# Optimization experiments

Measured on AMD Instinct MI355X. Metric: run time of the kernel, lower is better.

The kernel has to match this reference:

```python
import jax, jax.numpy as jnp
import numpy as np

B, T, I, H, O, L = 128, 512, 64, 256, 2, 2


def _gru_layer(x_seq, w_ih, w_hh, b_ih, b_hh):
    # x_seq: [B, T, in], w_ih: [3H, in], w_hh: [3H, H], biases: [3H]
    # PyTorch gate order: r, z, n
    xg = jnp.einsum('bti,gi->btg', x_seq, w_ih) + b_ih  # [B, T, 3H]
    h0 = jnp.zeros((x_seq.shape[0], w_hh.shape[1]), x_seq.dtype)

    def step(h, xg_t):
        hg = h @ w_hh.T + b_hh  # [B, 3H]
        xr, xz, xn = jnp.split(xg_t, 3, axis=-1)
        hr, hz, hn = jnp.split(hg, 3, axis=-1)
        r = jax.nn.sigmoid(xr + hr)
        z = jax.nn.sigmoid(xz + hz)
        n = jnp.tanh(xn + r * hn)
        h_new = (1.0 - z) * n + z * h
        return h_new, h_new

    _, hs = jax.lax.scan(step, h0, jnp.swapaxes(xg, 0, 1))  # [T, B, H]
    return jnp.swapaxes(hs, 0, 1)  # [B, T, H]


def setup_inputs() -> dict:
    key = jax.random.key(0)
    ks = jax.random.split(key, 12)
    s_ih0 = 1.0 / np.sqrt(H)
    inp = {
        'x': jax.random.normal(ks[0], (B, T, I), jnp.float32),
        'w_ih0': jax.random.uniform(ks[1], (3 * H, I), jnp.float32, -s_ih0, s_ih0),
        'w_hh0': jax.random.uniform(ks[2], (3 * H, H), jnp.float32, -s_ih0, s_ih0),
        'b_ih0': jax.random.uniform(ks[3], (3 * H,), jnp.float32, -s_ih0, s_ih0),
        'b_hh0': jax.random.uniform(ks[4], (3 * H,), jnp.float32, -s_ih0, s_ih0),
        'w_ih1': jax.random.uniform(ks[5], (3 * H, H), jnp.float32, -s_ih0, s_ih0),
        'w_hh1': jax.random.uniform(ks[6], (3 * H, H), jnp.float32, -s_ih0, s_ih0),
        'b_ih1': jax.random.uniform(ks[7], (3 * H,), jnp.float32, -s_ih0, s_ih0),
        'b_hh1': jax.random.uniform(ks[8], (3 * H,), jnp.float32, -s_ih0, s_ih0),
        'fc_w': jax.random.uniform(ks[9], (O, H), jnp.float32, -s_ih0, s_ih0),
        'fc_b': jax.random.uniform(ks[10], (O,), jnp.float32, -s_ih0, s_ih0),
    }
    return inp


def reference(x, w_ih0, w_hh0, b_ih0, b_hh0, w_ih1, w_hh1, b_ih1, b_hh1, fc_w, fc_b):
    h1 = _gru_layer(x, w_ih0, w_hh0, b_ih0, b_hh0)   # [B, T, H]
    h2 = _gru_layer(h1, w_ih1, w_hh1, b_ih1, b_hh1)  # [B, T, H]
    last = jax.nn.relu(h2[:, -1])                     # [B, H]
    return last @ fc_w.T + fc_b                       # [B, O]
```

## Files before the change

### kernel.cpp

```cpp
#include <hip/hip_runtime.h>


namespace {
constexpr int kB = 128, kT = 512, kI = 64, kH = 256, kBH = kB * kH;
constexpr int NG = 8, GW = 32, RPG = 16, NWG = 256, NT = 512;

constexpr int SRS = 36;
constexpr int SKS = 16 * SRS + 4;
constexpr int O_S0 = 0;
constexpr int O_S1 = O_S0 + 8 * SKS;
constexpr int O_X  = O_S1 + 8 * SKS;
constexpr int O_PB = O_X + RPG * 68;
constexpr int PBN  = 4 * 16 * 36;
constexpr int LDSF = O_PB + PBN;

constexpr int kFlagStride = 16;
}

__device__ __forceinline__ float sigf(float v) { return 1.0f / (1.0f + expf(-v)); }
__device__ __forceinline__ float dot4(const float4 a, const float4 b) {
  return a.x * b.x + a.y * b.y + a.z * b.z + a.w * b.w;
}
__device__ __forceinline__ float red8(float v) {
  v += __shfl_xor(v, 8);
  v += __shfl_xor(v, 16);
  v += __shfl_xor(v, 32);
  return v;
}
#define F4(p) (*(const float4*)(p))

__global__ __launch_bounds__(NT, 2) void gru_persistent(
    const float* __restrict__ x,
    const float* __restrict__ wih0, const float* __restrict__ whh0,
    const float* __restrict__ bih0, const float* __restrict__ bhh0,
    const float* __restrict__ wih1, const float* __restrict__ whh1,
    const float* __restrict__ bih1, const float* __restrict__ bhh1,
    const float* __restrict__ fcw, const float* __restrict__ fcb,
    float* __restrict__ h0buf, float* __restrict__ h1buf,
    unsigned* flags, float* __restrict__ out)
{
  __shared__ float lds[LDSF];

  const int bid = blockIdx.x;
  const int g   = bid >> 5;
  const int wg  = bid & (GW - 1);
  const int tid = threadIdx.x;
  const int r0  = g * RPG;
  const int j0  = wg * 8;

  const int wave = tid >> 6;
  const int lane = tid & 63;
  const int lay  = wave >> 2;
  const int fam  = (wave >> 1) & 1;
  const int rh   = wave & 1;
  const int ju   = lane & 7;
  const int ks   = lane >> 3;
  const int jg   = j0 + ju;

  for (int i = tid; i < PBN; i += NT) lds[O_PB + i] = 0.f;

  float4 wr0[8], wr1[8], wr2[8];
  if (lay == 0) {
    if (fam == 0) {
#define L0F0(wrg, gg) { \
      const float* wi = wih0 + (size_t)((gg) * kH + jg) * kI + ks * 8;   \
      const float* wh = whh0 + (size_t)((gg) * kH + jg) * kH + ks * 32;  \
      wrg[0] = F4(wi); wrg[1] = F4(wi + 4);                              \
      wrg[2] = F4(wh); wrg[3] = F4(wh + 4); wrg[4] = F4(wh + 8); }
      L0F0(wr0, 0) L0F0(wr1, 1) L0F0(wr2, 2)
    } else {
#define L0F1(wrg, gg) { \
      const float* wh = whh0 + (size_t)((gg) * kH + jg) * kH + ks * 32 + 12; \
      wrg[0] = F4(wh); wrg[1] = F4(wh + 4); wrg[2] = F4(wh + 8);             \
      wrg[3] = F4(wh + 12); wrg[4] = F4(wh + 16); }
      L0F1(wr0, 0) L0F1(wr1, 1) L0F1(wr2, 2)
    }
  } else {
    const float* ws = fam ? whh1 : wih1;
#define L1W(wrg, gg) { \
    const float* wp = ws + (size_t)((gg) * kH + jg) * kH + ks * 32;          \
    wrg[0] = F4(wp);      wrg[1] = F4(wp + 4);  wrg[2] = F4(wp + 8);         \
    wrg[3] = F4(wp + 12); wrg[4] = F4(wp + 16); wrg[5] = F4(wp + 20);        \
    wrg[6] = F4(wp + 24); wrg[7] = F4(wp + 28); }
    L1W(wr0, 0) L1W(wr1, 1) L1W(wr2, 2)
  }

  float fb_r = 0.f, fb_z = 0.f, fb_ni = 0.f, fb_nh = 0.f;
  if (tid < 256) {
    const int layf = tid >> 7, uf = tid & 7, jf = j0 + uf;
    const float* bi = layf ? bih1 : bih0;
    const float* bh = layf ? bhh1 : bhh0;
    fb_r  = bi[jf] + bh[jf];
    fb_z  = bi[kH + jf] + bh[kH + jf];
    fb_ni = bi[2 * kH + jf];
    fb_nh = bh[2 * kH + jf];
  }

  unsigned* myflag = flags + (unsigned)((g << 5) + (tid & 31)) * kFlagStride;

  __syncthreads();

  for (int s = 0; s <= kT; ++s) {
    {
      const float* h0p = h0buf + (size_t)((s + 1) & 1) * kBH;
      const float* h1p = h1buf + (size_t)(s & 1) * kBH;
      #pragma unroll
      for (int p = 0; p < 4; ++p) {
        const int i  = tid + p * NT;
        const int ro = i >> 7, k2 = i & 127;
        const int k  = k2 * 2, ksg = k >> 5, off = k & 31;
        const unsigned long long v0 = __hip_atomic_load(
            (const unsigned long long*)(h0p + (size_t)(r0 + ro) * kH) + k2,
            __ATOMIC_RELAXED, __HIP_MEMORY_SCOPE_AGENT);
        const unsigned long long v1 = __hip_atomic_load(
            (const unsigned long long*)(h1p + (size_t)(r0 + ro) * kH) + k2,
            __ATOMIC_RELAXED, __HIP_MEMORY_SCOPE_AGENT);
        float2 f0, f1;
        __builtin_memcpy(&f0, &v0, 8);
        __builtin_memcpy(&f1, &v1, 8);
        *(float2*)(lds + O_S0 + ksg * SKS + ro * SRS + off) = f0;
        *(float2*)(lds + O_S1 + ksg * SKS + ro * SRS + off) = f1;
      }
      if (s < kT && tid < 256) {
        const int ro = tid >> 4, c4 = (tid & 15) * 4;
        *(float4*)(lds + O_X + ro * 68 + c4) =
            F4(x + (size_t)(r0 + ro) * kT * kI + (size_t)s * kI + c4);
      }
    }
    __syncthreads();

    const bool wact = lay ? (s >= 1) : (s < kT);
    if (wact) {
      float prr[8], pzz[8], pni[8], pnh[8];
      #pragma unroll
      for (int r = 0; r < 8; ++r) {
        const int ro = rh * 8 + r;
        float pr = 0.f, pz = 0.f, pxi = 0.f, pxh = 0.f;
        if (lay == 0) {
          if (fam == 0) {
            const float* ax = lds + O_X + ro * 68 + ks * 8;
            const float4 x0 = F4(ax), x1 = F4(ax + 4);
            pr  += dot4(x0, wr0[0]) + dot4(x1, wr0[1]);
            pz  += dot4(x0, wr1[0]) + dot4(x1, wr1[1]);
            pxi += dot4(x0, wr2[0]) + dot4(x1, wr2[1]);
            const float* ah = lds + O_S0 + ks * SKS + ro * SRS;
            #pragma unroll
            for (int i = 0; i < 3; ++i) {
              const float4 hv = F4(ah + i * 4);
              pr  += dot4(hv, wr0[2 + i]);
              pz  += dot4(hv, wr1[2 + i]);
              pxh += dot4(hv, wr2[2 + i]);
            }
          } else {
            const float* ah = lds + O_S0 + ks * SKS + ro * SRS + 12;
            #pragma unroll
            for (int i = 0; i < 5; ++i) {
              const float4 hv = F4(ah + i * 4);
              pr  += dot4(hv, wr0[i]);
              pz  += dot4(hv, wr1[i]);
              pxh += dot4(hv, wr2[i]);
            }
          }
        } else {
          const float* aa = lds + (fam ? O_S1 : O_S0) + ks * SKS + ro * SRS;
          #pragma unroll
          for (int i = 0; i < 8; ++i) {
            const float4 av = F4(aa + i * 4);
            pr += dot4(av, wr0[i]);
            pz += dot4(av, wr1[i]);
            if (fam) pxh += dot4(av, wr2[i]);
            else     pxi += dot4(av, wr2[i]);
          }
        }
        prr[r] = pr; pzz[r] = pz; pni[r] = pxi; pnh[r] = pxh;
      }
      #pragma unroll
      for (int r = 0; r < 8; ++r) { prr[r] = red8(prr[r]); pzz[r] = red8(pzz[r]); }
      if (lay == 0 && fam == 0) {
        #pragma unroll
        for (int r = 0; r < 8; ++r) { pni[r] = red8(pni[r]); pnh[r] = red8(pnh[r]); }
      } else if (fam == 0) {
        #pragma unroll
        for (int r = 0; r < 8; ++r) pni[r] = red8(pni[r]);
      } else {
        #pragma unroll
        for (int r = 0; r < 8; ++r) pnh[r] = red8(pnh[r]);
      }
      if (ks == 0) {
        #pragma unroll
        for (int r = 0; r < 8; ++r) {
          float* pb = lds + O_PB + ((wave >> 1) * 16 + rh * 8 + r) * SRS + ju;
          pb[0] = prr[r]; pb[8] = pzz[r];
          if (lay == 0 && fam == 0) { pb[16] = pni[r]; pb[24] = pnh[r]; }
          else if (fam == 0)          pb[16] = pni[r];
          else                        pb[24] = pnh[r];
        }
      }
    }
    __syncthreads();

    if (tid < 256) {
      const int layf = tid >> 7;
      const bool act = layf ? (s >= 1) : (s < kT);
      if (act) {
        const int rof = (tid >> 3) & 15, uf = tid & 7, jf = j0 + uf;
        const float* p0 = lds + O_PB + ((layf * 2) * 16 + rof) * SRS + uf;
        const float* p1 = p0 + 16 * SRS;
        const float rr = sigf(p0[0] + p1[0] + fb_r);
        const float zz = sigf(p0[8] + p1[8] + fb_z);
        const float nn = tanhf(p0[16] + p1[16] + fb_ni +
                               rr * (p0[24] + p1[24] + fb_nh));
        const float hp = lds[(layf ? O_S1 : O_S0) +
                             (jf >> 5) * SKS + rof * SRS + (jf & 31)];
        const float hv = (1.f - zz) * nn + zz * hp;
        float* hout = layf ? (h1buf + (size_t)((s + 1) & 1) * kBH)
                           : (h0buf + (size_t)(s & 1) * kBH);
        __hip_atomic_store(hout + (size_t)(r0 + rof) * kH + jf, hv,
                           __ATOMIC_RELAXED, __HIP_MEMORY_SCOPE_AGENT);
      }
    }
    __syncthreads();

    if (tid == 0) {
      __hip_atomic_store(flags + (unsigned)bid * kFlagStride,
                         (unsigned)(s + 1),
                         __ATOMIC_RELAXED, __HIP_MEMORY_SCOPE_AGENT);
    }
    while (__hip_atomic_load(myflag, __ATOMIC_RELAXED,
                             __HIP_MEMORY_SCOPE_AGENT) < (unsigned)(s + 1)) {
      __builtin_amdgcn_s_sleep(1);
    }
    asm volatile("" ::: "memory");
  }

  if (wg == 0 && tid < 256) {
    const int rv = tid >> 4, o = (tid >> 3) & 1, kseg = tid & 7;
    const float* hf = h1buf + (size_t)kBH + (size_t)(r0 + rv) * kH;
    const float* wfc = fcw + (size_t)o * kH;
    float acc = 0.f;
    #pragma unroll 8
    for (int k = kseg * 32; k < kseg * 32 + 32; ++k) {
      const float hv = __hip_atomic_load(hf + k, __ATOMIC_RELAXED,
                                         __HIP_MEMORY_SCOPE_AGENT);
      acc += fmaxf(hv, 0.f) * wfc[k];
    }
    acc += __shfl_xor(acc, 1);
    acc += __shfl_xor(acc, 2);
    acc += __shfl_xor(acc, 4);
    if (kseg == 0) out[(r0 + rv) * 2 + o] = acc + fcb[o];
  }
}

extern "C" void kernel_launch(void* const* d_in, const int* in_sizes, int n_in,
                              void* d_out, int out_size, void* d_ws, size_t ws_size,
                              hipStream_t stream) {
  const float* x    = (const float*)d_in[0];
  const float* wih0 = (const float*)d_in[1];
  const float* whh0 = (const float*)d_in[2];
  const float* bih0 = (const float*)d_in[3];
  const float* bhh0 = (const float*)d_in[4];
  const float* wih1 = (const float*)d_in[5];
  const float* whh1 = (const float*)d_in[6];
  const float* bih1 = (const float*)d_in[7];
  const float* bhh1 = (const float*)d_in[8];
  const float* fcw  = (const float*)d_in[9];
  const float* fcb  = (const float*)d_in[10];

  float* h0buf = (float*)d_ws;
  float* h1buf = h0buf + 2 * kBH;
  unsigned* flags = (unsigned*)(h1buf + 2 * kBH);
  float* out = (float*)d_out;

  hipMemsetAsync(d_ws, 0,
                 (size_t)(4 * kBH) * sizeof(float) +
                 (size_t)NWG * kFlagStride * sizeof(unsigned), stream);

  gru_persistent<<<NWG, NT, 0, stream>>>(
      x, wih0, whh0, bih0, bhh0, wih1, whh1, bih1, bhh1,
      fcw, fcb, h0buf, h1buf, flags, out);
}
```

Before: 3.779 ms.

## Replace per-step flag barrier with tagged hidden-state words and triple buffering

Removes the end-of-step flag barrier that every workgroup spun on. Each stored hidden value now carries a 2-bit step tag in its low mantissa bits, and readers poll the data itself until the tags match. A third buffer slot lets producers run ahead, and a looser lagged flag only guards against slot reuse. This trades a full group barrier per step for data-driven waiting, at the cost of two bits of float precision and spin-polling on global loads.

After: 3.470 ms. 1.09x faster.

```diff
diff --git a/kernel.cpp b/kernel.cpp
--- a/kernel.cpp
+++ b/kernel.cpp
@@ -14,8 +14,10 @@
 constexpr int PBN  = 4 * 16 * 36;
 constexpr int LDSF = O_PB + PBN;
 
-constexpr int kFlagStride = 16;
-}
+constexpr int FS = 16;
+}
+
+using ull = unsigned long long;
 
 __device__ __forceinline__ float sigf(float v) { return 1.0f / (1.0f + expf(-v)); }
 __device__ __forceinline__ float dot4(const float4 a, const float4 b) {
@@ -36,8 +38,10 @@
     const float* __restrict__ wih1, const float* __restrict__ whh1,
     const float* __restrict__ bih1, const float* __restrict__ bhh1,
     const float* __restrict__ fcw, const float* __restrict__ fcb,
-    float* __restrict__ h0buf, float* __restrict__ h1buf,
-    unsigned* flags, float* __restrict__ out)
+    unsigned* __restrict__ h0w,
+    unsigned* __restrict__ h1w,
+    unsigned* __restrict__ sd,
+    float* __restrict__ out)
 {
   __shared__ float lds[LDSF];
 
@@ -96,38 +100,80 @@
     fb_nh = bh[2 * kH + jf];
   }
 
-  unsigned* myflag = flags + (unsigned)((g << 5) + (tid & 31)) * kFlagStride;
+  int RO[4], K2[4];
+  #pragma unroll
+  for (int p = 0; p < 4; ++p) {
+    const int i = tid + p * NT;
+    RO[p] = i >> 7; K2[p] = i & 127;
+  }
 
   __syncthreads();
 
   for (int s = 0; s <= kT; ++s) {
+    const int slot0 = (s + 2) % 3;
+    const int slot1 = (s + 1) % 3;
+    const unsigned e0 = (unsigned)(s & 3);
+    const unsigned e1 = (unsigned)((s - 1) & 3);
+
+    if (s < kT && tid < 256) {
+      const int ro = tid >> 4, c4 = (tid & 15) * 4;
+      *(float4*)(lds + O_X + ro * 68 + c4) =
+          F4(x + (size_t)(r0 + ro) * kT * kI + (size_t)s * kI + c4);
+    }
+    if (s >= 2 && tid >= 480) {
+      const unsigned* f = sd + (unsigned)((g << 5) + (tid - 480)) * FS;
+      while (__hip_atomic_load(f, __ATOMIC_RELAXED, __HIP_MEMORY_SCOPE_AGENT)
+             < (unsigned)(s - 1)) { }
+    }
+
+    ull v0[4], v1[4];
     {
-      const float* h0p = h0buf + (size_t)((s + 1) & 1) * kBH;
-      const float* h1p = h1buf + (size_t)(s & 1) * kBH;
+      const ull* A0[4]; const ull* A1[4];
       #pragma unroll
       for (int p = 0; p < 4; ++p) {
-        const int i  = tid + p * NT;
-        const int ro = i >> 7, k2 = i & 127;
-        const int k  = k2 * 2, ksg = k >> 5, off = k & 31;
-        const unsigned long long v0 = __hip_atomic_load(
-            (const unsigned long long*)(h0p + (size_t)(r0 + ro) * kH) + k2,
-            __ATOMIC_RELAXED, __HIP_MEMORY_SCOPE_AGENT);
-        const unsigned long long v1 = __hip_atomic_load(
-            (const unsigned long long*)(h1p + (size_t)(r0 + ro) * kH) + k2,
-            __ATOMIC_RELAXED, __HIP_MEMORY_SCOPE_AGENT);
-        float2 f0, f1;
-        __builtin_memcpy(&f0, &v0, 8);
-        __builtin_memcpy(&f1, &v1, 8);
-        *(float2*)(lds + O_S0 + ksg * SKS + ro * SRS + off) = f0;
+        A0[p] = (const ull*)(h0w + (size_t)slot0 * kBH +
+                             (size_t)(r0 + RO[p]) * kH) + K2[p];
+        A1[p] = (const ull*)(h1w + (size_t)slot1 * kBH +
+                             (size_t)(r0 + RO[p]) * kH) + K2[p];
+      }
+      for (;;) {
+        #pragma unroll
+        for (int p = 0; p < 4; ++p)
+          v0[p] = __hip_atomic_load(A0[p], __ATOMIC_RELAXED,
+                                    __HIP_MEMORY_SCOPE_AGENT);
+        if (s >= 1) {
+          #pragma unroll
+          for (int p = 0; p < 4; ++p)
+            v1[p] = __hip_atomic_load(A1[p], __ATOMIC_RELAXED,
+                                      __HIP_MEMORY_SCOPE_AGENT);
+        }
+        unsigned bad = 0;
+        #pragma unroll
+        for (int p = 0; p < 4; ++p)
+          bad |= ((unsigned)v0[p] ^ e0) | ((unsigned)(v0[p] >> 32) ^ e0);
+        if (s >= 1) {
+          #pragma unroll
+          for (int p = 0; p < 4; ++p)
+            bad |= ((unsigned)v1[p] ^ e1) | ((unsigned)(v1[p] >> 32) ^ e1);
+        }
+        if (!(bad & 3u)) break;
+      }
+    }
+    #pragma unroll
+    for (int p = 0; p < 4; ++p) {
+      const int ksg = K2[p] >> 4, off = (K2[p] * 2) & 31, ro = RO[p];
+      float2 f0; __builtin_memcpy(&f0, &v0[p], 8);
+      *(float2*)(lds + O_S0 + ksg * SKS + ro * SRS + off) = f0;
+      if (s >= 1) {
+        float2 f1; __builtin_memcpy(&f1, &v1[p], 8);
         *(float2*)(lds + O_S1 + ksg * SKS + ro * SRS + off) = f1;
       }
-      if (s < kT && tid < 256) {
-        const int ro = tid >> 4, c4 = (tid & 15) * 4;
-        *(float4*)(lds + O_X + ro * 68 + c4) =
-            F4(x + (size_t)(r0 + ro) * kT * kI + (size_t)s * kI + c4);
-      }
     }
     __syncthreads();
+    if (tid == 0) {
+      __hip_atomic_store(sd + (unsigned)bid * FS, (unsigned)(s + 1),
+                         __ATOMIC_RELAXED, __HIP_MEMORY_SCOPE_AGENT);
+    }
 
     const bool wact = lay ? (s >= 1) : (s < kT);
     if (wact) {
@@ -213,36 +259,31 @@
         const float hp = lds[(layf ? O_S1 : O_S0) +
                              (jf >> 5) * SKS + rof * SRS + (jf & 31)];
         const float hv = (1.f - zz) * nn + zz * hp;
-        float* hout = layf ? (h1buf + (size_t)((s + 1) & 1) * kBH)
-                           : (h0buf + (size_t)(s & 1) * kBH);
-        __hip_atomic_store(hout + (size_t)(r0 + rof) * kH + jf, hv,
-                           __ATOMIC_RELAXED, __HIP_MEMORY_SCOPE_AGENT);
+        const int slot = layf ? ((s - 1) % 3) : (s % 3);
+        const unsigned tag = layf ? (unsigned)(s & 3) : (unsigned)((s + 1) & 3);
+        const unsigned bits = (__float_as_uint(hv) & ~3u) | tag;
+        unsigned* hw = (layf ? h1w : h0w) + (size_t)slot * kBH +
+                       (size_t)(r0 + rof) * kH + jf;
+        __hip_atomic_store(hw, bits, __ATOMIC_RELAXED,
+                           __HIP_MEMORY_SCOPE_AGENT);
       }
     }
     __syncthreads();
-
-    if (tid == 0) {
-      __hip_atomic_store(flags + (unsigned)bid * kFlagStride,
-                         (unsigned)(s + 1),
-                         __ATOMIC_RELAXED, __HIP_MEMORY_SCOPE_AGENT);
-    }
-    while (__hip_atomic_load(myflag, __ATOMIC_RELAXED,
-                             __HIP_MEMORY_SCOPE_AGENT) < (unsigned)(s + 1)) {
-      __builtin_amdgcn_s_sleep(1);
-    }
-    asm volatile("" ::: "memory");
   }
 
   if (wg == 0 && tid < 256) {
     const int rv = tid >> 4, o = (tid >> 3) & 1, kseg = tid & 7;
-    const float* hf = h1buf + (size_t)kBH + (size_t)(r0 + rv) * kH;
+    const unsigned* hf = h1w + (size_t)((kT - 1) % 3) * kBH +
+                         (size_t)(r0 + rv) * kH;
     const float* wfc = fcw + (size_t)o * kH;
     float acc = 0.f;
-    #pragma unroll 8
     for (int k = kseg * 32; k < kseg * 32 + 32; ++k) {
-      const float hv = __hip_atomic_load(hf + k, __ATOMIC_RELAXED,
-                                         __HIP_MEMORY_SCOPE_AGENT);
-      acc += fmaxf(hv, 0.f) * wfc[k];
+      unsigned b;
+      do {
+        b = __hip_atomic_load(hf + k, __ATOMIC_RELAXED,
+                              __HIP_MEMORY_SCOPE_AGENT);
+      } while ((b & 3u) != (unsigned)(kT & 3));
+      acc += fmaxf(__uint_as_float(b), 0.f) * wfc[k];
     }
     acc += __shfl_xor(acc, 1);
     acc += __shfl_xor(acc, 2);
@@ -266,16 +307,16 @@
   const float* fcw  = (const float*)d_in[9];
   const float* fcb  = (const float*)d_in[10];
 
-  float* h0buf = (float*)d_ws;
-  float* h1buf = h0buf + 2 * kBH;
-  unsigned* flags = (unsigned*)(h1buf + 2 * kBH);
+  unsigned* h0w = (unsigned*)d_ws;
+  unsigned* h1w = h0w + 3 * kBH;
+  unsigned* sd  = h1w + 3 * kBH;
   float* out = (float*)d_out;
 
   hipMemsetAsync(d_ws, 0,
-                 (size_t)(4 * kBH) * sizeof(float) +
-                 (size_t)NWG * kFlagStride * sizeof(unsigned), stream);
+                 (size_t)(6 * kBH) * sizeof(unsigned) +
+                 (size_t)NWG * FS * sizeof(unsigned), stream);
 
   gru_persistent<<<NWG, NT, 0, stream>>>(
       x, wih0, whh0, bih0, bhh0, wih1, whh1, bih1, bhh1,
-      fcw, fcb, h0buf, h1buf, flags, out);
-}
+      fcw, fcb, h0w, h1w, sd, out);
+}
```

## Replace per-step flag barrier with tagged hidden-state words and row-chunk pipelining

Applied to the files above, without the earlier changes.

Replaces the group-wide flag barrier with data-carried synchronization. The low 2 bits of each stored hidden value hold a step tag, and readers spin until the tags they read match the expected step. Each timestep is split into 4 row-chunks, and the next chunk's h and x loads are issued before the current chunk's compute, overlapping global latency with math. A triple-buffered h slot and a loose slack flag (8 chunks behind) guard against buffer reuse. This trades two mantissa bits of precision and more frequent, smaller syncthreads phases for removing the full cross-workgroup barrier per step.

New measurement: 5.726 ms. 51.5% more time.

```diff
diff --git a/kernel.cpp b/kernel.cpp
--- a/kernel.cpp
+++ b/kernel.cpp
@@ -3,7 +3,7 @@
 
 namespace {
 constexpr int kB = 128, kT = 512, kI = 64, kH = 256, kBH = kB * kH;
-constexpr int NG = 8, GW = 32, RPG = 16, NWG = 256, NT = 512;
+constexpr int RPG = 16, NWG = 256, NT = 512;
 
 constexpr int SRS = 36;
 constexpr int SKS = 16 * SRS + 4;
@@ -14,8 +14,11 @@
 constexpr int PBN  = 4 * 16 * 36;
 constexpr int LDSF = O_PB + PBN;
 
-constexpr int kFlagStride = 16;
-}
+constexpr int FS = 16;
+}
+
+using ull = unsigned long long;
+using u32 = unsigned;
 
 __device__ __forceinline__ float sigf(float v) { return 1.0f / (1.0f + expf(-v)); }
 __device__ __forceinline__ float dot4(const float4 a, const float4 b) {
@@ -28,6 +31,8 @@
   return v;
 }
 #define F4(p) (*(const float4*)(p))
+#define AL(p)    __hip_atomic_load((p), __ATOMIC_RELAXED, __HIP_MEMORY_SCOPE_AGENT)
+#define AS(p, v) __hip_atomic_store((p), (v), __ATOMIC_RELAXED, __HIP_MEMORY_SCOPE_AGENT)
 
 __global__ __launch_bounds__(NT, 2) void gru_persistent(
     const float* __restrict__ x,
@@ -36,20 +41,21 @@
     const float* __restrict__ wih1, const float* __restrict__ whh1,
     const float* __restrict__ bih1, const float* __restrict__ bhh1,
     const float* __restrict__ fcw, const float* __restrict__ fcb,
-    float* __restrict__ h0buf, float* __restrict__ h1buf,
-    unsigned* flags, float* __restrict__ out)
+    u32* __restrict__ h0w,
+    u32* __restrict__ h1w,
+    u32* __restrict__ sd,
+    float* __restrict__ out)
 {
   __shared__ float lds[LDSF];
 
   const int bid = blockIdx.x;
   const int g   = bid >> 5;
-  const int wg  = bid & (GW - 1);
+  const int wg  = bid & 31;
   const int tid = threadIdx.x;
   const int r0  = g * RPG;
   const int j0  = wg * 8;
 
-  const int wave = tid >> 6;
-  const int lane = tid & 63;
+  const int wave = tid >> 6, lane = tid & 63;
   const int lay  = wave >> 2;
   const int fam  = (wave >> 1) & 1;
   const int rh   = wave & 1;
@@ -85,164 +91,201 @@
     L1W(wr0, 0) L1W(wr1, 1) L1W(wr2, 2)
   }
 
-  float fb_r = 0.f, fb_z = 0.f, fb_ni = 0.f, fb_nh = 0.f;
-  if (tid < 256) {
-    const int layf = tid >> 7, uf = tid & 7, jf = j0 + uf;
+  float fb_r = 0.f, fb_z = 0.f, fn_i = 0.f, fn_h = 0.f;
+  if (tid < 64) {
+    const int layf = tid >> 5, uf = tid & 7, jf = j0 + uf;
     const float* bi = layf ? bih1 : bih0;
     const float* bh = layf ? bhh1 : bhh0;
-    fb_r  = bi[jf] + bh[jf];
-    fb_z  = bi[kH + jf] + bh[kH + jf];
-    fb_ni = bi[2 * kH + jf];
-    fb_nh = bh[2 * kH + jf];
-  }
-
-  unsigned* myflag = flags + (unsigned)((g << 5) + (tid & 31)) * kFlagStride;
-
+    fb_r = bi[jf] + bh[jf];
+    fb_z = bi[kH + jf] + bh[kH + jf];
+    fn_i = bi[2 * kH + jf];
+    fn_h = bh[2 * kH + jf];
+  }
+
+  u32* sdp = sd + (u32)bid * FS;
+  const int sro = tid >> 7, sk2 = tid & 127;
+
+  {
+    const ull* a0 = (const ull*)(h0w + (size_t)2 * kBH +
+                                 (size_t)(r0 + sro) * kH) + sk2;
+    ull v0 = AL(a0);
+    while ((((u32)v0 | (u32)(v0 >> 32)) & 3u)) {
+      __builtin_amdgcn_s_sleep(1);
+      v0 = AL(a0);
+    }
+    const int ksg = sk2 >> 4, off = (sk2 * 2) & 31;
+    float2 f0; __builtin_memcpy(&f0, &v0, 8);
+    *(float2*)(lds + O_S0 + ksg * SKS + sro * SRS + off) = f0;
+    if (tid < 64) {
+      const int rx = tid >> 4, c4 = (tid & 15) * 4;
+      *(float4*)(lds + O_X + rx * 68 + c4) =
+          F4(x + (size_t)(r0 + rx) * kT * kI + c4);
+    }
+  }
   __syncthreads();
 
   for (int s = 0; s <= kT; ++s) {
-    {
-      const float* h0p = h0buf + (size_t)((s + 1) & 1) * kBH;
-      const float* h1p = h1buf + (size_t)(s & 1) * kBH;
-      #pragma unroll
-      for (int p = 0; p < 4; ++p) {
-        const int i  = tid + p * NT;
-        const int ro = i >> 7, k2 = i & 127;
-        const int k  = k2 * 2, ksg = k >> 5, off = k & 31;
-        const unsigned long long v0 = __hip_atomic_load(
-            (const unsigned long long*)(h0p + (size_t)(r0 + ro) * kH) + k2,
-            __ATOMIC_RELAXED, __HIP_MEMORY_SCOPE_AGENT);
-        const unsigned long long v1 = __hip_atomic_load(
-            (const unsigned long long*)(h1p + (size_t)(r0 + ro) * kH) + k2,
-            __ATOMIC_RELAXED, __HIP_MEMORY_SCOPE_AGENT);
-        float2 f0, f1;
-        __builtin_memcpy(&f0, &v0, 8);
-        __builtin_memcpy(&f1, &v1, 8);
-        *(float2*)(lds + O_S0 + ksg * SKS + ro * SRS + off) = f0;
-        *(float2*)(lds + O_S1 + ksg * SKS + ro * SRS + off) = f1;
-      }
-      if (s < kT && tid < 256) {
-        const int ro = tid >> 4, c4 = (tid & 15) * 4;
-        *(float4*)(lds + O_X + ro * 68 + c4) =
-            F4(x + (size_t)(r0 + ro) * kT * kI + (size_t)s * kI + c4);
-      }
-    }
-    __syncthreads();
-
-    const bool wact = lay ? (s >= 1) : (s < kT);
-    if (wact) {
-      float prr[8], pzz[8], pni[8], pnh[8];
-      #pragma unroll
-      for (int r = 0; r < 8; ++r) {
-        const int ro = rh * 8 + r;
-        float pr = 0.f, pz = 0.f, pxi = 0.f, pxh = 0.f;
-        if (lay == 0) {
-          if (fam == 0) {
-            const float* ax = lds + O_X + ro * 68 + ks * 8;
-            const float4 x0 = F4(ax), x1 = F4(ax + 4);
-            pr  += dot4(x0, wr0[0]) + dot4(x1, wr0[1]);
-            pz  += dot4(x0, wr1[0]) + dot4(x1, wr1[1]);
-            pxi += dot4(x0, wr2[0]) + dot4(x1, wr2[1]);
-            const float* ah = lds + O_S0 + ks * SKS + ro * SRS;
-            #pragma unroll
-            for (int i = 0; i < 3; ++i) {
-              const float4 hv = F4(ah + i * 4);
-              pr  += dot4(hv, wr0[2 + i]);
-              pz  += dot4(hv, wr1[2 + i]);
-              pxh += dot4(hv, wr2[2 + i]);
+    for (int m = 0; m < 4; ++m) {
+      const int K  = s * 4 + m;
+      const int m2 = (m + 1) & 3;
+      const int s2 = (m == 3) ? s + 1 : s;
+      const bool dostage = (s2 <= kT);
+
+      if (tid == 0) AS(sdp, (u32)(K + 1));
+      if (K >= 8 && tid >= 480) {
+        const u32* f = sd + (u32)((g << 5) + (tid - 480)) * FS;
+        while ((int)AL(f) < K - 7) __builtin_amdgcn_s_sleep(1);
+      }
+
+      ull v0 = 0, v1 = 0; float4 xpf = {};
+      const ull *a0 = nullptr, *a1 = nullptr;
+      if (dostage) {
+        const int ro2 = m2 * 4 + sro;
+        a0 = (const ull*)(h0w + (size_t)((s2 + 2) % 3) * kBH +
+                          (size_t)(r0 + ro2) * kH) + sk2;
+        v0 = AL(a0);
+        if (s2 >= 1) {
+          a1 = (const ull*)(h1w + (size_t)((s2 + 1) % 3) * kBH +
+                            (size_t)(r0 + ro2) * kH) + sk2;
+          v1 = AL(a1);
+        }
+        if (tid < 64 && s2 < kT) {
+          const int rx = m2 * 4 + (tid >> 4), c4 = (tid & 15) * 4;
+          xpf = F4(x + (size_t)(r0 + rx) * kT * kI + (size_t)s2 * kI + c4);
+        }
+      }
+
+      const bool wact = lay ? (s >= 1) : (s < kT);
+      if (wact) {
+        float prr[2], pzz[2], pni[2], pnh[2];
+        #pragma unroll
+        for (int r = 0; r < 2; ++r) {
+          const int ro = m * 4 + rh * 2 + r;
+          float pr = 0.f, pz = 0.f, pxi = 0.f, pxh = 0.f;
+          if (lay == 0) {
+            if (fam == 0) {
+              const float* ax = lds + O_X + ro * 68 + ks * 8;
+              const float4 x0 = F4(ax), x1 = F4(ax + 4);
+              pr  += dot4(x0, wr0[0]) + dot4(x1, wr0[1]);
+              pz  += dot4(x0, wr1[0]) + dot4(x1, wr1[1]);
+              pxi += dot4(x0, wr2[0]) + dot4(x1, wr2[1]);
+              const float* ah = lds + O_S0 + ks * SKS + ro * SRS;
+              #pragma unroll
+              for (int i = 0; i < 3; ++i) {
+                const float4 hv = F4(ah + i * 4);
+                pr  += dot4(hv, wr0[2 + i]);
+                pz  += dot4(hv, wr1[2 + i]);
+                pxh += dot4(hv, wr2[2 + i]);
+              }
+            } else {
+              const float* ah = lds + O_S0 + ks * SKS + ro * SRS + 12;
+              #pragma unroll
+              for (int i = 0; i < 5; ++i) {
+                const float4 hv = F4(ah + i * 4);
+                pr  += dot4(hv, wr0[i]);
+                pz  += dot4(hv, wr1[i]);
+                pxh += dot4(hv, wr2[i]);
+              }
             }
           } else {
-            const float* ah = lds + O_S0 + ks * SKS + ro * SRS + 12;
+            const float* aa = lds + (fam ? O_S1 : O_S0) + ks * SKS + ro * SRS;
             #pragma unroll
-            for (int i = 0; i < 5; ++i) {
-              const float4 hv = F4(ah + i * 4);
-              pr  += dot4(hv, wr0[i]);
-              pz  += dot4(hv, wr1[i]);
-              pxh += dot4(hv, wr2[i]);
+            for (int i = 0; i < 8; ++i) {
+              const float4 av = F4(aa + i * 4);
+              pr += dot4(av, wr0[i]);
+              pz += dot4(av, wr1[i]);
+              if (fam) pxh += dot4(av, wr2[i]);
+              else     pxi += dot4(av, wr2[i]);
             }
           }
+          prr[r] = pr; pzz[r] = pz; pni[r] = pxi; pnh[r] = pxh;
+        }
+        #pragma unroll
+        for (int r = 0; r < 2; ++r) { prr[r] = red8(prr[r]); pzz[r] = red8(pzz[r]); }
+        if (lay == 0 && fam == 0) {
+          #pragma unroll
+          for (int r = 0; r < 2; ++r) { pni[r] = red8(pni[r]); pnh[r] = red8(pnh[r]); }
+        } else if (fam == 0) {
+          #pragma unroll
+          for (int r = 0; r < 2; ++r) pni[r] = red8(pni[r]);
         } else {
-          const float* aa = lds + (fam ? O_S1 : O_S0) + ks * SKS + ro * SRS;
           #pragma unroll
-          for (int i = 0; i < 8; ++i) {
-            const float4 av = F4(aa + i * 4);
-            pr += dot4(av, wr0[i]);
-            pz += dot4(av, wr1[i]);
-            if (fam) pxh += dot4(av, wr2[i]);
-            else     pxi += dot4(av, wr2[i]);
+          for (int r = 0; r < 2; ++r) pnh[r] = red8(pnh[r]);
+        }
+        if (ks == 0) {
+          #pragma unroll
+          for (int r = 0; r < 2; ++r) {
+            const int ro = m * 4 + rh * 2 + r;
+            float* pb = lds + O_PB + ((wave >> 1) * 16 + ro) * SRS + ju;
+            pb[0] = prr[r]; pb[8] = pzz[r];
+            if (lay == 0 && fam == 0) { pb[16] = pni[r]; pb[24] = pnh[r]; }
+            else if (fam == 0)          pb[16] = pni[r];
+            else                        pb[24] = pnh[r];
           }
         }
-        prr[r] = pr; pzz[r] = pz; pni[r] = pxi; pnh[r] = pxh;
-      }
-      #pragma unroll
-      for (int r = 0; r < 8; ++r) { prr[r] = red8(prr[r]); pzz[r] = red8(pzz[r]); }
-      if (lay == 0 && fam == 0) {
-        #pragma unroll
-        for (int r = 0; r < 8; ++r) { pni[r] = red8(pni[r]); pnh[r] = red8(pnh[r]); }
-      } else if (fam == 0) {
-        #pragma unroll
-        for (int r = 0; r < 8; ++r) pni[r] = red8(pni[r]);
-      } else {
-        #pragma unroll
-        for (int r = 0; r < 8; ++r) pnh[r] = red8(pnh[r]);
-      }
-      if (ks == 0) {
-        #pragma unroll
-        for (int r = 0; r < 8; ++r) {
-          float* pb = lds + O_PB + ((wave >> 1) * 16 + rh * 8 + r) * SRS + ju;
-          pb[0] = prr[r]; pb[8] = pzz[r];
-          if (lay == 0 && fam == 0) { pb[16] = pni[r]; pb[24] = pnh[r]; }
-          else if (fam == 0)          pb[16] = pni[r];
-          else                        pb[24] = pnh[r];
-        }
-      }
-    }
-    __syncthreads();
-
-    if (tid < 256) {
-      const int layf = tid >> 7;
-      const bool act = layf ? (s >= 1) : (s < kT);
-      if (act) {
-        const int rof = (tid >> 3) & 15, uf = tid & 7, jf = j0 + uf;
-        const float* p0 = lds + O_PB + ((layf * 2) * 16 + rof) * SRS + uf;
-        const float* p1 = p0 + 16 * SRS;
-        const float rr = sigf(p0[0] + p1[0] + fb_r);
-        const float zz = sigf(p0[8] + p1[8] + fb_z);
-        const float nn = tanhf(p0[16] + p1[16] + fb_ni +
-                               rr * (p0[24] + p1[24] + fb_nh));
-        const float hp = lds[(layf ? O_S1 : O_S0) +
-                             (jf >> 5) * SKS + rof * SRS + (jf & 31)];
-        const float hv = (1.f - zz) * nn + zz * hp;
-        float* hout = layf ? (h1buf + (size_t)((s + 1) & 1) * kBH)
-                           : (h0buf + (size_t)(s & 1) * kBH);
-        __hip_atomic_store(hout + (size_t)(r0 + rof) * kH + jf, hv,
-                           __ATOMIC_RELAXED, __HIP_MEMORY_SCOPE_AGENT);
-      }
-    }
-    __syncthreads();
-
-    if (tid == 0) {
-      __hip_atomic_store(flags + (unsigned)bid * kFlagStride,
-                         (unsigned)(s + 1),
-                         __ATOMIC_RELAXED, __HIP_MEMORY_SCOPE_AGENT);
-    }
-    while (__hip_atomic_load(myflag, __ATOMIC_RELAXED,
-                             __HIP_MEMORY_SCOPE_AGENT) < (unsigned)(s + 1)) {
-      __builtin_amdgcn_s_sleep(1);
-    }
-    asm volatile("" ::: "memory");
+      }
+      __syncthreads();
+
+      if (tid < 64) {
+        const int layf = tid >> 5;
+        const bool act = layf ? (s >= 1) : (s < kT);
+        if (act) {
+          const int local = tid & 31, rof = m * 4 + (local >> 3), uf = local & 7;
+          const int jf = j0 + uf;
+          const float* p0 = lds + O_PB + ((layf * 2) * 16 + rof) * SRS + uf;
+          const float* p1 = p0 + 16 * SRS;
+          const float rr = sigf(p0[0] + p1[0] + fb_r);
+          const float zz = sigf(p0[8] + p1[8] + fb_z);
+          const float nn = tanhf(p0[16] + p1[16] + fn_i +
+                                 rr * (p0[24] + p1[24] + fn_h));
+          const float hp = lds[(layf ? O_S1 : O_S0) +
+                               (jf >> 5) * SKS + rof * SRS + (jf & 31)];
+          const float hv = (1.f - zz) * nn + zz * hp;
+          const int slot = layf ? ((s - 1) % 3) : (s % 3);
+          const u32 tag = layf ? (u32)(s & 3) : (u32)((s + 1) & 3);
+          const u32 bits = (__float_as_uint(hv) & ~3u) | tag;
+          u32* hw = (layf ? h1w : h0w) + (size_t)slot * kBH +
+                    (size_t)(r0 + rof) * kH + jf;
+          AS(hw, bits);
+        }
+      }
+      if (dostage) {
+        const u32 e0 = (u32)(s2 & 3), e1 = (u32)((s2 - 1) & 3);
+        for (;;) {
+          u32 bad = ((u32)v0 ^ e0) | ((u32)(v0 >> 32) ^ e0);
+          if (s2 >= 1) bad |= ((u32)v1 ^ e1) | ((u32)(v1 >> 32) ^ e1);
+          if (!(bad & 3u)) break;
+          __builtin_amdgcn_s_sleep(1);
+          v0 = AL(a0);
+          if (s2 >= 1) v1 = AL(a1);
+        }
+        const int ro2 = m2 * 4 + sro, ksg = sk2 >> 4, off = (sk2 * 2) & 31;
+        float2 f0; __builtin_memcpy(&f0, &v0, 8);
+        *(float2*)(lds + O_S0 + ksg * SKS + ro2 * SRS + off) = f0;
+        if (s2 >= 1) {
+          float2 f1; __builtin_memcpy(&f1, &v1, 8);
+          *(float2*)(lds + O_S1 + ksg * SKS + ro2 * SRS + off) = f1;
+        }
+        if (tid < 64 && s2 < kT) {
+          const int rx = m2 * 4 + (tid >> 4), c4 = (tid & 15) * 4;
+          *(float4*)(lds + O_X + rx * 68 + c4) = xpf;
+        }
+      }
+      __syncthreads();
+    }
   }
 
   if (wg == 0 && tid < 256) {
     const int rv = tid >> 4, o = (tid >> 3) & 1, kseg = tid & 7;
-    const float* hf = h1buf + (size_t)kBH + (size_t)(r0 + rv) * kH;
+    const u32* hf = h1w + (size_t)((kT - 1) % 3) * kBH + (size_t)(r0 + rv) * kH;
     const float* wfc = fcw + (size_t)o * kH;
     float acc = 0.f;
-    #pragma unroll 8
     for (int k = kseg * 32; k < kseg * 32 + 32; ++k) {
-      const float hv = __hip_atomic_load(hf + k, __ATOMIC_RELAXED,
-                                         __HIP_MEMORY_SCOPE_AGENT);
-      acc += fmaxf(hv, 0.f) * wfc[k];
+      u32 b;
+      do {
+        b = AL(hf + k);
+      } while ((b & 3u) != (u32)(kT & 3));
+      acc += fmaxf(__uint_as_float(b), 0.f) * wfc[k];
     }
     acc += __shfl_xor(acc, 1);
     acc += __shfl_xor(acc, 2);
@@ -266,16 +309,16 @@
   const float* fcw  = (const float*)d_in[9];
   const float* fcb  = (const float*)d_in[10];
 
-  float* h0buf = (float*)d_ws;
-  float* h1buf = h0buf + 2 * kBH;
-  unsigned* flags = (unsigned*)(h1buf + 2 * kBH);
+  u32* h0w = (u32*)d_ws;
+  u32* h1w = h0w + 3 * kBH;
+  u32* sd  = h1w + 3 * kBH;
   float* out = (float*)d_out;
 
   hipMemsetAsync(d_ws, 0,
-                 (size_t)(4 * kBH) * sizeof(float) +
-                 (size_t)NWG * kFlagStride * sizeof(unsigned), stream);
+                 (size_t)(6 * kBH) * sizeof(u32) +
+                 (size_t)NWG * FS * sizeof(u32), stream);
 
   gru_persistent<<<NWG, NT, 0, stream>>>(
       x, wih0, whh0, bih0, bhh0, wih1, whh1, bih1, bhh1,
-      fcw, fcb, h0buf, h1buf, flags, out);
-}
+      fcw, fcb, h0w, h1w, sd, out);
+}
```
